# Performance work log

Measured on AMD Instinct MI355X. Metric: run time of the kernel, lower is better.

Reference implementation:

```python
import jax, jax.numpy as jnp
import numpy as np

D_MODEL = 1024
D_FF = 4096
LN_EPS = 1e-5


def _layer_norm(x, gamma, beta):
    mu = jnp.mean(x, axis=-1, keepdims=True)
    var = jnp.mean(jnp.square(x - mu), axis=-1, keepdims=True)
    return (x - mu) * jax.lax.rsqrt(var + LN_EPS) * gamma + beta


def setup_inputs() -> dict:
    key = jax.random.key(0)
    ks = jax.random.split(key, 16)
    B, S, D, F = 2, 2048, D_MODEL, D_FF
    s_d = 1.0 / np.sqrt(D)
    s_f = 1.0 / np.sqrt(F)
    u = lambda k, shape, s: jax.random.uniform(k, shape, jnp.float32, -s, s)
    return {
        "x": jax.random.normal(ks[0], (B, S, D), jnp.float32),
        "wq": u(ks[1], (D, D), s_d), "bq": u(ks[2], (D,), s_d),
        "wk": u(ks[3], (D, D), s_d), "bk": u(ks[4], (D,), s_d),
        "wv": u(ks[5], (D, D), s_d), "bv": u(ks[6], (D,), s_d),
        "wo": u(ks[7], (D, D), s_d), "bo": u(ks[8], (D,), s_d),
        "w1": u(ks[9], (F, D), s_d), "b1": u(ks[10], (F,), s_d),
        "w2": u(ks[11], (D, F), s_f), "b2": u(ks[12], (D,), s_f),
        "g1": jnp.ones((D,), jnp.float32), "be1": jnp.zeros((D,), jnp.float32),
        "g2": jnp.ones((D,), jnp.float32), "be2": jnp.zeros((D,), jnp.float32),
        "num_heads": 16,
    }


def reference(x, wq, bq, wk, bk, wv, bv, wo, bo, w1, b1, w2, b2, g1, be1, g2, be2, num_heads):
    B, S, D = x.shape
    H = num_heads
    dk = D // H
    scale = 1.0 / np.sqrt(dk)

    # --- self-attention (pre-norm) ---
    h = _layer_norm(x, g1, be1)
    q = (h @ wq.T + bq).reshape(B, S, H, dk)
    k = (h @ wk.T + bk).reshape(B, S, H, dk)
    v = (h @ wv.T + bv).reshape(B, S, H, dk)
    scores = jnp.einsum("bqhd,bkhd->bhqk", q, k) * scale  # [B,H,S,S]
    attn = jax.nn.softmax(scores, axis=-1)
    ctx = jnp.einsum("bhqk,bkhd->bqhd", attn, v).reshape(B, S, D)
    x = x + ctx @ wo.T + bo

    # --- feed-forward (pre-norm, exact GELU as in torch default) ---
    h = _layer_norm(x, g2, be2)
    h = jax.nn.gelu(h @ w1.T + b1, approximate=False)
    x = x + h @ w2.T + b2
    return x
```

## Files before the change

kernel.cpp:

```cpp
#include <hip/hip_runtime.h>

typedef __attribute__((ext_vector_type(8))) __bf16 bf16x8;
typedef __attribute__((ext_vector_type(4))) __bf16 bf16x4;
typedef __attribute__((ext_vector_type(4))) float floatx4;
typedef void __attribute__((address_space(3))) lds_void_t;
typedef const void __attribute__((address_space(1))) gbl_void_t;

#define D_MODEL 1024
#define SEQ     2048
#define BATCH   2
#define NH      16
#define DK      64
#define DFF     4096
#define NTOK    (BATCH * SEQ)
#define QKVS    3072

__device__ __forceinline__ float gelu_exact(float x) {
    return 0.5f * x * (1.0f + erff(x * 0.70710678118654752f));
}

__global__ __launch_bounds__(256) void cast_f32_bf16(const float* __restrict__ src,
                                                     __bf16* __restrict__ dst, int n) {
    int i = (blockIdx.x * 256 + threadIdx.x) * 8;
    if (i >= n) return;
    floatx4 a = *(const floatx4*)(src + i);
    floatx4 b = *(const floatx4*)(src + i + 4);
    bf16x8 o;
    for (int j = 0; j < 4; ++j) { o[j] = (__bf16)a[j]; o[4 + j] = (__bf16)b[j]; }
    *(bf16x8*)(dst + i) = o;
}

__global__ __launch_bounds__(64) void ln_kernel(const float* __restrict__ x,
                                                const float* __restrict__ g,
                                                const float* __restrict__ b,
                                                __bf16* __restrict__ out) {
    int row = blockIdx.x, lane = threadIdx.x, base = lane * 16;
    const float* xr = x + (size_t)row * D_MODEL + base;
    float v[16];
    for (int j = 0; j < 4; ++j) {
        floatx4 a = *(const floatx4*)(xr + 4 * j);
        for (int i = 0; i < 4; ++i) v[4 * j + i] = a[i];
    }
    float s = 0.f, sq = 0.f;
    for (int i = 0; i < 16; ++i) { s += v[i]; sq += v[i] * v[i]; }
    for (int o = 1; o < 64; o <<= 1) { s += __shfl_xor(s, o); sq += __shfl_xor(sq, o); }
    float mu = s * (1.0f / D_MODEL);
    float var = sq * (1.0f / D_MODEL) - mu * mu;
    float rstd = rsqrtf(fmaxf(var, 0.f) + 1e-5f);

    const floatx4* gp = (const floatx4*)(g + base);
    const floatx4* bp = (const floatx4*)(b + base);
    bf16x8 o0, o1;
    for (int j = 0; j < 2; ++j) {
        floatx4 gv0 = gp[2 * j], gv1 = gp[2 * j + 1];
        floatx4 bv0 = bp[2 * j], bv1 = bp[2 * j + 1];
        for (int i = 0; i < 4; ++i) {
            float r0 = (v[8 * j + i] - mu) * rstd * gv0[i] + bv0[i];
            float r1 = (v[8 * j + 4 + i] - mu) * rstd * gv1[i] + bv1[i];
            if (j == 0) { o0[i] = (__bf16)r0; o0[4 + i] = (__bf16)r1; }
            else        { o1[i] = (__bf16)r0; o1[4 + i] = (__bf16)r1; }
        }
    }
    bf16x8* op = (bf16x8*)(out + (size_t)row * D_MODEL + base);
    op[0] = o0; op[1] = o1;
}

template <typename OutT, bool GELU, bool TRIBIAS>
__global__ __launch_bounds__(256) void gemm_bt(const __bf16* __restrict__ A,
                                               const __bf16* __restrict__ W,
                                               const float* __restrict__ bias0,
                                               const float* __restrict__ bias1,
                                               const float* __restrict__ bias2,
                                               const float* __restrict__ res,
                                               OutT* __restrict__ out,
                                               int M, int N, int K) {
    __shared__ __bf16 As[128][32];
    __shared__ __bf16 Ws[128][32];

    int m0 = blockIdx.y * 128, n0 = blockIdx.x * 128;
    int t = threadIdx.x;
    int lane = t & 63, wave = t >> 6;
    int wm = (wave >> 1) * 64, wn = (wave & 1) * 64;
    int fr = lane & 15, quad = lane >> 4;
    int srow = t >> 2, scol = (t & 3) * 8;

    floatx4 acc[4][4] = {};

    const __bf16* Ab = A + (size_t)(m0 + srow) * K + scol;
    const __bf16* Wb = W + (size_t)(n0 + srow) * K + scol;
    lds_void_t* lA0 = (lds_void_t*)&As[wave * 16][0];
    lds_void_t* lA1 = (lds_void_t*)&As[64 + wave * 16][0];
    lds_void_t* lW0 = (lds_void_t*)&Ws[wave * 16][0];
    lds_void_t* lW1 = (lds_void_t*)&Ws[64 + wave * 16][0];

    for (int k0 = 0; k0 < K; k0 += 32) {
        __syncthreads();
        __builtin_amdgcn_global_load_lds((gbl_void_t*)(Ab + k0), lA0, 16, 0, 0);
        __builtin_amdgcn_global_load_lds((gbl_void_t*)(Ab + (size_t)64 * K + k0), lA1, 16, 0, 0);
        __builtin_amdgcn_global_load_lds((gbl_void_t*)(Wb + k0), lW0, 16, 0, 0);
        __builtin_amdgcn_global_load_lds((gbl_void_t*)(Wb + (size_t)64 * K + k0), lW1, 16, 0, 0);
        __syncthreads();

        bf16x8 af[4], wf[4];
        for (int i = 0; i < 4; ++i) af[i] = *(const bf16x8*)&As[wm + i * 16 + fr][quad * 8];
        for (int i = 0; i < 4; ++i) wf[i] = *(const bf16x8*)&Ws[wn + i * 16 + fr][quad * 8];
        for (int mi = 0; mi < 4; ++mi)
            for (int ni = 0; ni < 4; ++ni)
                acc[mi][ni] = __builtin_amdgcn_mfma_f32_16x16x32_bf16(af[mi], wf[ni], acc[mi][ni], 0, 0, 0);
    }

    for (int ni = 0; ni < 4; ++ni) {
        int col = n0 + wn + ni * 16 + fr;
        const float* bp = bias0;
        int bcol = col;
        if (TRIBIAS) { bp = col < 1024 ? bias0 : (col < 2048 ? bias1 : bias2); bcol = col & 1023; }
        float bv = bp[bcol];
        for (int mi = 0; mi < 4; ++mi) {
            for (int r = 0; r < 4; ++r) {
                int row = m0 + wm + mi * 16 + quad * 4 + r;
                float v = acc[mi][ni][r] + bv;
                if (GELU) v = gelu_exact(v);
                if (res) v += res[(size_t)row * N + col];
                out[(size_t)row * N + col] = (OutT)v;
            }
        }
    }
}

__global__ __launch_bounds__(256) void transpose_v(const __bf16* __restrict__ qkv,
                                                   __bf16* __restrict__ vt) {
    __shared__ __bf16 tile[64][72];
    int b = blockIdx.z, h = blockIdx.y, s0 = blockIdx.x * 64;
    int t = threadIdx.x;
    int dl = (t & 7) * 8, sl = t >> 3;
    for (int p = 0; p < 2; ++p) {
        int s = sl + p * 32;
        bf16x8 val = *(const bf16x8*)(qkv + (size_t)(b * SEQ + s0 + s) * QKVS + 2048 + h * DK + dl);
        *(bf16x8*)&tile[s][dl] = val;
    }
    __syncthreads();
    int sl2 = (t & 7) * 8, d = t >> 3;
    for (int p = 0; p < 2; ++p) {
        int dd = d + p * 32;
        bf16x8 val;
        for (int j = 0; j < 8; ++j) val[j] = tile[sl2 + j][dd];
        *(bf16x8*)(vt + ((size_t)(b * NH + h) * DK + dd) * SEQ + s0 + sl2) = val;
    }
}

__global__ __launch_bounds__(256, 2) void attn_kernel(const __bf16* __restrict__ qkv,
                                                      const __bf16* __restrict__ vt,
                                                      __bf16* __restrict__ ctx) {
    __shared__ __bf16 Klds[128][64];
    __shared__ __bf16 Vlds[64][128];
    __shared__ __bf16 Plds[4][16][136];
    int b = blockIdx.z, h = blockIdx.y;
    int wave = threadIdx.x >> 6, lane = threadIdx.x & 63;
    int q0 = blockIdx.x * 64 + wave * 16;
    int fr = lane & 15, quad = lane >> 4;
    const float scale = 0.125f;

    const __bf16* qp = qkv + (size_t)(b * SEQ + q0 + fr) * QKVS + h * DK + quad * 8;
    bf16x8 qf0 = *(const bf16x8*)qp;
    bf16x8 qf1 = *(const bf16x8*)(qp + 32);

    const __bf16* kg = qkv + (size_t)b * SEQ * QKVS + 1024 + h * DK;
    const __bf16* vg = vt + (size_t)(b * NH + h) * DK * SEQ;

    int krow = wave * 8 + (lane >> 3);
    int kcbp = (lane & 7) * 16;
    int vrow = wave * 4 + (lane >> 4);
    int vcbp = (lane & 15) * 16;
    int swb = (fr & 7) << 4;

    floatx4 o[4] = {};
    float m_i = -1e30f, l_i = 0.f;

#pragma unroll
    for (int p = 0; p < 4; ++p) {
        int kr = krow + p * 32;
        int vr = vrow + p * 16;
        __builtin_amdgcn_global_load_lds(
            (gbl_void_t*)(kg + (size_t)kr * QKVS + ((kcbp ^ ((kr & 7) << 4)) >> 1)),
            (lds_void_t*)&Klds[p * 32 + wave * 8][0], 16, 0, 0);
        __builtin_amdgcn_global_load_lds(
            (gbl_void_t*)(vg + (size_t)vr * SEQ + ((vcbp ^ ((vr & 7) << 4)) >> 1)),
            (lds_void_t*)&Vlds[p * 16 + wave * 4][0], 16, 0, 0);
    }
    __syncthreads();

    for (int k0 = 0; k0 < SEQ; k0 += 128) {
        bf16x8 kA[8], kB[8];
#pragma unroll
        for (int f = 0; f < 8; ++f) {
            const char* rp = (const char*)&Klds[0][0] + (f * 16 + fr) * 128;
            kA[f] = *(const bf16x8*)(rp + ((quad * 16) ^ swb));
            kB[f] = *(const bf16x8*)(rp + ((64 + quad * 16) ^ swb));
        }
        bf16x8 vf[4][4];
#pragma unroll
        for (int c = 0; c < 4; ++c)
#pragma unroll
            for (int ti = 0; ti < 4; ++ti)
                vf[c][ti] = *(const bf16x8*)((const char*)&Vlds[0][0] +
                                             (ti * 16 + fr) * 256 + ((c * 64 + quad * 16) ^ swb));
        __syncthreads();

        if (k0 + 128 < SEQ) {
#pragma unroll
            for (int p = 0; p < 4; ++p) {
                int kr = krow + p * 32;
                int vr = vrow + p * 16;
                __builtin_amdgcn_global_load_lds(
                    (gbl_void_t*)(kg + (size_t)(k0 + 128 + kr) * QKVS + ((kcbp ^ ((kr & 7) << 4)) >> 1)),
                    (lds_void_t*)&Klds[p * 32 + wave * 8][0], 16, 0, 0);
                __builtin_amdgcn_global_load_lds(
                    (gbl_void_t*)(vg + (size_t)vr * SEQ + k0 + 128 + ((vcbp ^ ((vr & 7) << 4)) >> 1)),
                    (lds_void_t*)&Vlds[p * 16 + wave * 4][0], 16, 0, 0);
            }
        }

        floatx4 s[8];
#pragma unroll
        for (int f = 0; f < 8; ++f) {
            floatx4 z = {0.f, 0.f, 0.f, 0.f};
            z = __builtin_amdgcn_mfma_f32_16x16x32_bf16(kA[f], qf0, z, 0, 0, 0);
            s[f] = __builtin_amdgcn_mfma_f32_16x16x32_bf16(kB[f], qf1, z, 0, 0, 0);
        }

        float mx = s[0][0];
#pragma unroll
        for (int f = 0; f < 8; ++f)
#pragma unroll
            for (int r = 0; r < 4; ++r) mx = fmaxf(mx, s[f][r]);
        mx *= scale;
        mx = fmaxf(mx, __shfl_xor(mx, 16));
        mx = fmaxf(mx, __shfl_xor(mx, 32));
        float mn = fmaxf(m_i, mx);
        float alpha = __expf(m_i - mn);
        m_i = mn;
        float rs = 0.f;
#pragma unroll
        for (int f = 0; f < 8; ++f) {
            bf16x4 pk;
#pragma unroll
            for (int r = 0; r < 4; ++r) {
                float p = __expf(s[f][r] * scale - mn);
                rs += p;
                pk[r] = (__bf16)p;
            }
            *(bf16x4*)&Plds[wave][fr][f * 16 + quad * 4] = pk;
        }
        rs += __shfl_xor(rs, 16);
        rs += __shfl_xor(rs, 32);
        l_i = l_i * alpha + rs;
        float aB[4];
#pragma unroll
        for (int r = 0; r < 4; ++r) aB[r] = __shfl(alpha, quad * 4 + r);
#pragma unroll
        for (int ti = 0; ti < 4; ++ti)
#pragma unroll
            for (int r = 0; r < 4; ++r) o[ti][r] *= aB[r];
        __threadfence_block();

        bf16x8 pa[4];
#pragma unroll
        for (int c = 0; c < 4; ++c)
            pa[c] = *(const bf16x8*)&Plds[wave][fr][c * 32 + quad * 8];
#pragma unroll
        for (int c = 0; c < 4; ++c)
#pragma unroll
            for (int ti = 0; ti < 4; ++ti)
                o[ti] = __builtin_amdgcn_mfma_f32_16x16x32_bf16(pa[c], vf[c][ti], o[ti], 0, 0, 0);
        __threadfence_block();

        __syncthreads();
    }
    float lB[4];
#pragma unroll
    for (int r = 0; r < 4; ++r) lB[r] = __shfl(l_i, quad * 4 + r);
#pragma unroll
    for (int ti = 0; ti < 4; ++ti)
#pragma unroll
        for (int r = 0; r < 4; ++r)
            ctx[(size_t)(b * SEQ + q0 + quad * 4 + r) * D_MODEL + h * DK + ti * 16 + fr] =
                (__bf16)(o[ti][r] / lB[r]);
}

extern "C" void kernel_launch(void* const* d_in, const int* in_sizes, int n_in,
                              void* d_out, int out_size, void* d_ws, size_t ws_size,
                              hipStream_t stream) {
    const float* x   = (const float*)d_in[0];
    const float* wq  = (const float*)d_in[1];
    const float* bq  = (const float*)d_in[2];
    const float* wk  = (const float*)d_in[3];
    const float* bk  = (const float*)d_in[4];
    const float* wv  = (const float*)d_in[5];
    const float* bv  = (const float*)d_in[6];
    const float* wo  = (const float*)d_in[7];
    const float* bo  = (const float*)d_in[8];
    const float* w1  = (const float*)d_in[9];
    const float* b1  = (const float*)d_in[10];
    const float* w2  = (const float*)d_in[11];
    const float* b2  = (const float*)d_in[12];
    const float* g1  = (const float*)d_in[13];
    const float* be1 = (const float*)d_in[14];
    const float* g2  = (const float*)d_in[15];
    const float* be2 = (const float*)d_in[16];
    float* out = (float*)d_out;

    char* ws = (char*)d_ws;
    const size_t MB = 1024 * 1024;
    __bf16* wqkvB = (__bf16*)(ws);
    __bf16* woB   = (__bf16*)(ws + 6 * MB);
    __bf16* w1B   = (__bf16*)(ws + 8 * MB);
    __bf16* w2B   = (__bf16*)(ws + 16 * MB);
    __bf16* h1    = (__bf16*)(ws + 24 * MB);
    float*  x1    = (float*)(ws + 24 * MB);
    __bf16* qkv   = (__bf16*)(ws + 40 * MB);
    __bf16* vt    = (__bf16*)(ws + 64 * MB);
    __bf16* ffh   = (__bf16*)(ws + 40 * MB);
    __bf16* ctx   = (__bf16*)d_out;
    __bf16* h2    = (__bf16*)d_out;

    const int NDD = D_MODEL * D_MODEL;
    const int NDF = D_MODEL * DFF;
    cast_f32_bf16<<<NDD / 2048, 256, 0, stream>>>(wq, wqkvB, NDD);
    cast_f32_bf16<<<NDD / 2048, 256, 0, stream>>>(wk, wqkvB + NDD, NDD);
    cast_f32_bf16<<<NDD / 2048, 256, 0, stream>>>(wv, wqkvB + 2 * NDD, NDD);
    cast_f32_bf16<<<NDD / 2048, 256, 0, stream>>>(wo, woB, NDD);
    cast_f32_bf16<<<NDF / 2048, 256, 0, stream>>>(w1, w1B, NDF);
    cast_f32_bf16<<<NDF / 2048, 256, 0, stream>>>(w2, w2B, NDF);

    dim3 gQKV(QKVS / 128, NTOK / 128);
    dim3 gD(D_MODEL / 128, NTOK / 128);
    dim3 gF(DFF / 128, NTOK / 128);
    dim3 gAttn(SEQ / 64, NH, BATCH);

    ln_kernel<<<NTOK, 64, 0, stream>>>(x, g1, be1, h1);
    gemm_bt<__bf16, false, true><<<gQKV, 256, 0, stream>>>(h1, wqkvB, bq, bk, bv, nullptr, qkv, NTOK, QKVS, D_MODEL);
    transpose_v<<<gAttn, 256, 0, stream>>>(qkv, vt);
    attn_kernel<<<gAttn, 256, 0, stream>>>(qkv, vt, ctx);
    gemm_bt<float, false, false><<<gD, 256, 0, stream>>>(ctx, woB, bo, bo, bo, x, x1, NTOK, D_MODEL, D_MODEL);
    ln_kernel<<<NTOK, 64, 0, stream>>>(x1, g2, be2, h2);
    gemm_bt<__bf16, true, false><<<gF, 256, 0, stream>>>(h2, w1B, b1, b1, b1, nullptr, ffh, NTOK, DFF, D_MODEL);
    gemm_bt<float, false, false><<<gD, 256, 0, stream>>>(ffh, w2B, b2, b2, b2, x1, out, NTOK, D_MODEL, DFF);
}
```

Measured before the change: 487.3 us.

## Double-buffer GEMM LDS tiles and split-K the N=1024 GEMMs with reduce kernel

The GEMM kernel now double-buffers its LDS tiles, issuing the next k-step's global-to-LDS loads before computing on the current buffer, and drops one barrier per iteration. The two output projections with N=1024 (Wo and W2) get a two-way split-K over blockIdx.z. Each half writes fp32 partials, and a new reduce kernel adds the partials, the bias and the residual. The split doubles the block count for these GEMMs, which otherwise launch only 256 blocks on a many-CU GPU. The cost is extra partial-sum memory traffic, an extra launch, and workspace aliasing, including writing a partial into d_out.

```diff
diff --git a/kernel.cpp b/kernel.cpp
--- a/kernel.cpp
+++ b/kernel.cpp
@@ -65,17 +65,17 @@
     op[0] = o0; op[1] = o1;
 }
 
-template <typename OutT, bool GELU, bool TRIBIAS>
+template <typename OutT, bool GELU, bool TRIBIAS, int KSPLIT>
 __global__ __launch_bounds__(256) void gemm_bt(const __bf16* __restrict__ A,
                                                const __bf16* __restrict__ W,
                                                const float* __restrict__ bias0,
                                                const float* __restrict__ bias1,
                                                const float* __restrict__ bias2,
                                                const float* __restrict__ res,
-                                               OutT* __restrict__ out,
+                                               OutT* out, float* part1,
                                                int M, int N, int K) {
-    __shared__ __bf16 As[128][32];
-    __shared__ __bf16 Ws[128][32];
+    __shared__ __bf16 As[2][128][32];
+    __shared__ __bf16 Ws[2][128][32];
 
     int m0 = blockIdx.y * 128, n0 = blockIdx.x * 128;
     int t = threadIdx.x;
@@ -84,47 +84,94 @@
     int fr = lane & 15, quad = lane >> 4;
     int srow = t >> 2, scol = (t & 3) * 8;
 
+    int Ks = K / KSPLIT;
+    int kbeg = (KSPLIT > 1) ? blockIdx.z * Ks : 0;
+
     floatx4 acc[4][4] = {};
 
-    const __bf16* Ab = A + (size_t)(m0 + srow) * K + scol;
-    const __bf16* Wb = W + (size_t)(n0 + srow) * K + scol;
-    lds_void_t* lA0 = (lds_void_t*)&As[wave * 16][0];
-    lds_void_t* lA1 = (lds_void_t*)&As[64 + wave * 16][0];
-    lds_void_t* lW0 = (lds_void_t*)&Ws[wave * 16][0];
-    lds_void_t* lW1 = (lds_void_t*)&Ws[64 + wave * 16][0];
-
-    for (int k0 = 0; k0 < K; k0 += 32) {
+    const __bf16* Ab = A + (size_t)(m0 + srow) * K + kbeg + scol;
+    const __bf16* Wb = W + (size_t)(n0 + srow) * K + kbeg + scol;
+
+    auto stage = [&](int buf, int k0) {
+        __builtin_amdgcn_global_load_lds((gbl_void_t*)(Ab + k0),
+                                         (lds_void_t*)&As[buf][wave * 16][0], 16, 0, 0);
+        __builtin_amdgcn_global_load_lds((gbl_void_t*)(Ab + (size_t)64 * K + k0),
+                                         (lds_void_t*)&As[buf][64 + wave * 16][0], 16, 0, 0);
+        __builtin_amdgcn_global_load_lds((gbl_void_t*)(Wb + k0),
+                                         (lds_void_t*)&Ws[buf][wave * 16][0], 16, 0, 0);
+        __builtin_amdgcn_global_load_lds((gbl_void_t*)(Wb + (size_t)64 * K + k0),
+                                         (lds_void_t*)&Ws[buf][64 + wave * 16][0], 16, 0, 0);
+    };
+
+    stage(0, 0);
+    int nsteps = Ks / 32;
+    for (int s = 0; s < nsteps; ++s) {
+        int cur = s & 1;
         __syncthreads();
-        __builtin_amdgcn_global_load_lds((gbl_void_t*)(Ab + k0), lA0, 16, 0, 0);
-        __builtin_amdgcn_global_load_lds((gbl_void_t*)(Ab + (size_t)64 * K + k0), lA1, 16, 0, 0);
-        __builtin_amdgcn_global_load_lds((gbl_void_t*)(Wb + k0), lW0, 16, 0, 0);
-        __builtin_amdgcn_global_load_lds((gbl_void_t*)(Wb + (size_t)64 * K + k0), lW1, 16, 0, 0);
-        __syncthreads();
+        if (s + 1 < nsteps) stage(cur ^ 1, (s + 1) * 32);
 
         bf16x8 af[4], wf[4];
-        for (int i = 0; i < 4; ++i) af[i] = *(const bf16x8*)&As[wm + i * 16 + fr][quad * 8];
-        for (int i = 0; i < 4; ++i) wf[i] = *(const bf16x8*)&Ws[wn + i * 16 + fr][quad * 8];
+#pragma unroll
+        for (int i = 0; i < 4; ++i) af[i] = *(const bf16x8*)&As[cur][wm + i * 16 + fr][quad * 8];
+#pragma unroll
+        for (int i = 0; i < 4; ++i) wf[i] = *(const bf16x8*)&Ws[cur][wn + i * 16 + fr][quad * 8];
+#pragma unroll
         for (int mi = 0; mi < 4; ++mi)
+#pragma unroll
             for (int ni = 0; ni < 4; ++ni)
                 acc[mi][ni] = __builtin_amdgcn_mfma_f32_16x16x32_bf16(af[mi], wf[ni], acc[mi][ni], 0, 0, 0);
     }
 
-    for (int ni = 0; ni < 4; ++ni) {
-        int col = n0 + wn + ni * 16 + fr;
-        const float* bp = bias0;
-        int bcol = col;
-        if (TRIBIAS) { bp = col < 1024 ? bias0 : (col < 2048 ? bias1 : bias2); bcol = col & 1023; }
-        float bv = bp[bcol];
-        for (int mi = 0; mi < 4; ++mi) {
-            for (int r = 0; r < 4; ++r) {
-                int row = m0 + wm + mi * 16 + quad * 4 + r;
-                float v = acc[mi][ni][r] + bv;
-                if (GELU) v = gelu_exact(v);
-                if (res) v += res[(size_t)row * N + col];
-                out[(size_t)row * N + col] = (OutT)v;
+    if (KSPLIT > 1) {
+        float* pb = (blockIdx.z == 0) ? (float*)out : part1;
+#pragma unroll
+        for (int ni = 0; ni < 4; ++ni) {
+            int col = n0 + wn + ni * 16 + fr;
+#pragma unroll
+            for (int mi = 0; mi < 4; ++mi)
+#pragma unroll
+                for (int r = 0; r < 4; ++r) {
+                    int row = m0 + wm + mi * 16 + quad * 4 + r;
+                    pb[(size_t)row * N + col] = acc[mi][ni][r];
+                }
+        }
+    } else {
+#pragma unroll
+        for (int ni = 0; ni < 4; ++ni) {
+            int col = n0 + wn + ni * 16 + fr;
+            const float* bp = bias0;
+            int bcol = col;
+            if (TRIBIAS) { bp = col < 1024 ? bias0 : (col < 2048 ? bias1 : bias2); bcol = col & 1023; }
+            float bv = bp[bcol];
+#pragma unroll
+            for (int mi = 0; mi < 4; ++mi) {
+#pragma unroll
+                for (int r = 0; r < 4; ++r) {
+                    int row = m0 + wm + mi * 16 + quad * 4 + r;
+                    float v = acc[mi][ni][r] + bv;
+                    if (GELU) v = gelu_exact(v);
+                    if (res) v += res[(size_t)row * N + col];
+                    out[(size_t)row * N + col] = (OutT)v;
+                }
             }
         }
     }
+}
+
+__global__ __launch_bounds__(256) void reduce_k2(const float* __restrict__ p0,
+                                                 const float* p1,
+                                                 const float* __restrict__ res,
+                                                 const float* __restrict__ bias,
+                                                 float* out) {
+    int i = (blockIdx.x * 256 + threadIdx.x) * 4;
+    floatx4 a = *(const floatx4*)(p0 + i);
+    floatx4 b = *(const floatx4*)(p1 + i);
+    floatx4 r = *(const floatx4*)(res + i);
+    floatx4 bv = *(const floatx4*)(bias + (i & 1023));
+    floatx4 o;
+#pragma unroll
+    for (int j = 0; j < 4; ++j) o[j] = a[j] + b[j] + r[j] + bv[j];
+    *(floatx4*)(out + i) = o;
 }
 
 __global__ __launch_bounds__(256) void transpose_v(const __bf16* __restrict__ qkv,
@@ -320,6 +367,9 @@
     __bf16* qkv   = (__bf16*)(ws + 40 * MB);
     __bf16* vt    = (__bf16*)(ws + 64 * MB);
     __bf16* ffh   = (__bf16*)(ws + 40 * MB);
+    float*  pA0   = (float*)(ws + 40 * MB);
+    float*  pA1   = (float*)(ws + 56 * MB);
+    float*  pF0   = (float*)(ws);
     __bf16* ctx   = (__bf16*)d_out;
     __bf16* h2    = (__bf16*)d_out;
 
@@ -333,16 +383,19 @@
     cast_f32_bf16<<<NDF / 2048, 256, 0, stream>>>(w2, w2B, NDF);
 
     dim3 gQKV(QKVS / 128, NTOK / 128);
-    dim3 gD(D_MODEL / 128, NTOK / 128);
+    dim3 gDz(D_MODEL / 128, NTOK / 128, 2);
     dim3 gF(DFF / 128, NTOK / 128);
     dim3 gAttn(SEQ / 64, NH, BATCH);
+    int gRed = NTOK * D_MODEL / (256 * 4);
 
     ln_kernel<<<NTOK, 64, 0, stream>>>(x, g1, be1, h1);
-    gemm_bt<__bf16, false, true><<<gQKV, 256, 0, stream>>>(h1, wqkvB, bq, bk, bv, nullptr, qkv, NTOK, QKVS, D_MODEL);
+    gemm_bt<__bf16, false, true, 1><<<gQKV, 256, 0, stream>>>(h1, wqkvB, bq, bk, bv, nullptr, qkv, nullptr, NTOK, QKVS, D_MODEL);
     transpose_v<<<gAttn, 256, 0, stream>>>(qkv, vt);
     attn_kernel<<<gAttn, 256, 0, stream>>>(qkv, vt, ctx);
-    gemm_bt<float, false, false><<<gD, 256, 0, stream>>>(ctx, woB, bo, bo, bo, x, x1, NTOK, D_MODEL, D_MODEL);
+    gemm_bt<float, false, false, 2><<<gDz, 256, 0, stream>>>(ctx, woB, nullptr, nullptr, nullptr, nullptr, pA0, pA1, NTOK, D_MODEL, D_MODEL);
+    reduce_k2<<<gRed, 256, 0, stream>>>(pA0, pA1, x, bo, x1);
     ln_kernel<<<NTOK, 64, 0, stream>>>(x1, g2, be2, h2);
-    gemm_bt<__bf16, true, false><<<gF, 256, 0, stream>>>(h2, w1B, b1, b1, b1, nullptr, ffh, NTOK, DFF, D_MODEL);
-    gemm_bt<float, false, false><<<gD, 256, 0, stream>>>(ffh, w2B, b2, b2, b2, x1, out, NTOK, D_MODEL, DFF);
-}
+    gemm_bt<__bf16, true, false, 1><<<gF, 256, 0, stream>>>(h2, w1B, b1, b1, b1, nullptr, ffh, nullptr, NTOK, DFF, D_MODEL);
+    gemm_bt<float, false, false, 2><<<gDz, 256, 0, stream>>>(ffh, w2B, nullptr, nullptr, nullptr, nullptr, pF0, (float*)d_out, NTOK, D_MODEL, DFF);
+    reduce_k2<<<gRed, 256, 0, stream>>>(pF0, (float*)d_out, x1, b2, out);
+}
```

Measured after the change: 432.5 us. 11.2% less time.
